# Kernel optimization log

Hardware: AMD Instinct MI355X
Metric: run time of the kernel (lower is better)

## Reference

```python
import jax, jax.numpy as jnp
import numpy as np
from jax import lax

STRIDE = 6  # from init_kwargs


def setup_inputs() -> dict:
    key = jax.random.key(0)
    # spike-like activations in [0, 1); feature maps [F, H, W]
    s = jax.random.uniform(key, (128, 384, 384), dtype=jnp.float32)
    return {"s": s}


def reference(s):
    # Faithful to PoolingConnection.compute: for output (k, i, j) it takes
    #   max(s[k, i*stride : i*stride + h, j*stride : j*stride + w])
    # where h = H // stride, w = W // stride (NOT pooling_size -- that arg
    # is unused in the original code). Python slicing clips at the array
    # boundary, which equals right/bottom padding with -inf under a max.
    F, H, W = s.shape
    h, w = H // STRIDE, W // STRIDE
    pad_h = (h - 1) * STRIDE + h - H  # so that output height == h
    pad_w = (w - 1) * STRIDE + w - W
    out = lax.reduce_window(
        s,
        -jnp.inf,
        lax.max,
        window_dimensions=(1, h, w),
        window_strides=(1, STRIDE, STRIDE),
        padding=[(0, 0), (0, pad_h), (0, pad_w)],
    )  # [F, h, w]
    return out
```

## Files before the change

### kernel.cpp

```cpp
#include <hip/hip_runtime.h>
#include <math.h>


constexpr int F  = 128;
constexpr int H  = 384;
constexpr int W  = 384;
constexpr int ST = 6;
constexpr int OH = 64;
constexpr int OW = 64;

constexpr int NSEG   = 37;
constexpr int SEGPAD = NSEG + 10;

#define NINF (-__builtin_huge_valf())

__device__ __forceinline__ float sh_ninf(float v, int lane, int d) {
    float r = __shfl(v, lane + d, 64);
    return (lane + d > 63) ? NINF : r;
}

__device__ __forceinline__ float slide_window(float m, float p3, int lane) {
    const float a1 = fmaxf(m,  sh_ninf(m,  lane, 1));
    const float a2 = fmaxf(a1, sh_ninf(a1, lane, 2));
    const float a3 = fmaxf(a2, sh_ninf(a2, lane, 4));
    const float a4 = fmaxf(a3, sh_ninf(a1, lane, 8));
    return fmaxf(a4, sh_ninf(p3, lane, 10));
}

__global__ __launch_bounds__(1024) void pool_fused_kernel(const float* __restrict__ s,
                                                          float* __restrict__ out) {
    __shared__ float segm[SEGPAD][64];
    __shared__ float segp[SEGPAD][64];

    const int k    = blockIdx.x >> 1;
    const int half = blockIdx.x & 1;

    const int sbeg = half ? 27 : 0;
    const int obeg = half ? 27 : 0;
    const int ni   = half ? 37 : 27;

    const int tid  = threadIdx.x;
    const int wv   = tid >> 6;
    const int lane = tid & 63;

    for (int job = tid; job < 10 * 64; job += 1024) {
        const int g = NSEG + (job >> 6);
        const int j = job & 63;
        segm[g][j] = NINF;
        segp[g][j] = NINF;
    }

    const float* base = s + ((size_t)k * H + sbeg * ST) * W + lane * 6;
    for (int gl = wv; gl < NSEG; gl += 16) {
        const float* seg = base + (size_t)gl * ST * W;
        float vm6 = NINF, vp6 = NINF;
        float vm4 = NINF, vp4 = NINF;
        #pragma unroll
        for (int t = 0; t < 6; ++t) {
            const float* row = seg + (size_t)t * W;
            const float2 e0 = *reinterpret_cast<const float2*>(row);
            const float2 e1 = *reinterpret_cast<const float2*>(row + 2);
            const float2 e2 = *reinterpret_cast<const float2*>(row + 4);
            const float p3 = fmaxf(fmaxf(e0.x, e0.y), fmaxf(e1.x, e1.y));
            const float m  = fmaxf(p3, fmaxf(e2.x, e2.y));
            vm6 = fmaxf(vm6, m);
            vp6 = fmaxf(vp6, p3);
            if (t < 4) { vm4 = fmaxf(vm4, m); vp4 = fmaxf(vp4, p3); }
        }
        segm[gl][lane] = slide_window(vm6, vp6, lane);
        segp[gl][lane] = slide_window(vm4, vp4, lane);
    }
    __syncthreads();

    for (int job = tid; job < ni * 64; job += 1024) {
        const int li = job >> 6;
        const int j  = job & 63;
        float acc = segp[li + 10][j];
        #pragma unroll
        for (int t = 0; t < 10; ++t) acc = fmaxf(acc, segm[li + t][j]);
        out[((size_t)k * OH + obeg + li) * OW + j] = acc;
    }
}

extern "C" void kernel_launch(void* const* d_in, const int* in_sizes, int n_in,
                              void* d_out, int out_size, void* d_ws, size_t ws_size,
                              hipStream_t stream) {
    const float* s = (const float*)d_in[0];
    float* out     = (float*)d_out;
    pool_fused_kernel<<<F * 2, 1024, 0, stream>>>(s, out);
}
```

Measured before the change: 18.54 us.

## Split segment work evenly across halves and fix up boundary rows in second kernel

```diff
diff --git a/kernel.cpp b/kernel.cpp
--- a/kernel.cpp
+++ b/kernel.cpp
@@ -8,9 +8,6 @@
 constexpr int ST = 6;
 constexpr int OH = 64;
 constexpr int OW = 64;
-
-constexpr int NSEG   = 37;
-constexpr int SEGPAD = NSEG + 10;
 
 #define NINF (-__builtin_huge_valf())
 
@@ -27,31 +24,32 @@
     return fmaxf(a4, sh_ninf(p3, lane, 10));
 }
 
-__global__ __launch_bounds__(1024) void pool_fused_kernel(const float* __restrict__ s,
-                                                          float* __restrict__ out) {
-    __shared__ float segm[SEGPAD][64];
-    __shared__ float segp[SEGPAD][64];
+__global__ __launch_bounds__(1024) void pool_main(const float* __restrict__ s,
+                                                  float* __restrict__ out,
+                                                  float* __restrict__ ws_m,
+                                                  float* __restrict__ ws_p) {
+    __shared__ float segm[42][64];
+    __shared__ float segp[42][64];
 
     const int k    = blockIdx.x >> 1;
     const int half = blockIdx.x & 1;
-
-    const int sbeg = half ? 27 : 0;
-    const int obeg = half ? 27 : 0;
-    const int ni   = half ? 37 : 27;
+    const int sbeg = half * 32;
 
     const int tid  = threadIdx.x;
     const int wv   = tid >> 6;
     const int lane = tid & 63;
 
     for (int job = tid; job < 10 * 64; job += 1024) {
-        const int g = NSEG + (job >> 6);
+        const int g = 32 + (job >> 6);
         const int j = job & 63;
         segm[g][j] = NINF;
         segp[g][j] = NINF;
     }
 
     const float* base = s + ((size_t)k * H + sbeg * ST) * W + lane * 6;
-    for (int gl = wv; gl < NSEG; gl += 16) {
+    #pragma unroll
+    for (int it = 0; it < 2; ++it) {
+        const int gl = wv + it * 16;
         const float* seg = base + (size_t)gl * ST * W;
         float vm6 = NINF, vp6 = NINF;
         float vm4 = NINF, vp4 = NINF;
@@ -72,6 +70,21 @@
     }
     __syncthreads();
 
+    if (!half) {
+        for (int job = tid; job < 10 * 64; job += 1024) {
+            const int g = job >> 6, c = job & 63;
+            ws_m[((size_t)k * 20 + g) * 64 + c] = segm[22 + g][c];
+        }
+    } else {
+        for (int job = tid; job < 20 * 64; job += 1024) {
+            const int g = job >> 6, c = job & 63;
+            if (g < 10) ws_m[((size_t)k * 20 + 10 + g) * 64 + c] = segm[g][c];
+            else        ws_p[((size_t)k * 10 + (g - 10)) * 64 + c] = segp[g - 10][c];
+        }
+    }
+
+    const int obeg = half ? 32 : 0;
+    const int ni   = half ? 32 : 22;
     for (int job = tid; job < ni * 64; job += 1024) {
         const int li = job >> 6;
         const int j  = job & 63;
@@ -82,10 +95,31 @@
     }
 }
 
+__global__ __launch_bounds__(256) void pool_fixup(const float* __restrict__ ws_m,
+                                                  const float* __restrict__ ws_p,
+                                                  float* __restrict__ out) {
+    const int gtid = blockIdx.x * 256 + threadIdx.x;
+    const int wid  = gtid >> 6;
+    const int lane = gtid & 63;
+    if (wid >= F * 10) return;
+    const int k = wid / 10;
+    const int r = wid % 10;
+
+    const float* m = ws_m + ((size_t)k * 20 + r) * 64 + lane;
+    float acc = ws_p[((size_t)k * 10 + r) * 64 + lane];
+    #pragma unroll
+    for (int t = 0; t < 10; ++t) acc = fmaxf(acc, m[(size_t)t * 64]);
+    out[((size_t)k * OH + 22 + r) * OW + lane] = acc;
+}
+
 extern "C" void kernel_launch(void* const* d_in, const int* in_sizes, int n_in,
                               void* d_out, int out_size, void* d_ws, size_t ws_size,
                               hipStream_t stream) {
     const float* s = (const float*)d_in[0];
     float* out     = (float*)d_out;
-    pool_fused_kernel<<<F * 2, 1024, 0, stream>>>(s, out);
+    float* ws_m    = (float*)d_ws;
+    float* ws_p    = ws_m + (size_t)F * 20 * 64;
+
+    pool_main<<<F * 2, 1024, 0, stream>>>(s, out, ws_m, ws_p);
+    pool_fixup<<<(F * 10 * 64 + 255) / 256, 256, 0, stream>>>(ws_m, ws_p, out);
 }
```

Result: slower. 19.37 us (+4.5%).

## Load rows with coalesced float4 and redistribute columns through LDS

Applied to the files above, without the earlier changes.

```diff
diff --git a/kernel.cpp b/kernel.cpp
--- a/kernel.cpp
+++ b/kernel.cpp
@@ -27,14 +27,28 @@
     return fmaxf(a4, sh_ninf(p3, lane, 10));
 }
 
+__device__ __forceinline__ float4 fmax4(float4 a, float4 b) {
+    float4 r;
+    r.x = fmaxf(a.x, b.x); r.y = fmaxf(a.y, b.y);
+    r.z = fmaxf(a.z, b.z); r.w = fmaxf(a.w, b.w);
+    return r;
+}
+
+__device__ __forceinline__ float2 fmax2f(float2 a, float2 b) {
+    float2 r; r.x = fmaxf(a.x, b.x); r.y = fmaxf(a.y, b.y); return r;
+}
+
 __global__ __launch_bounds__(1024) void pool_fused_kernel(const float* __restrict__ s,
                                                           float* __restrict__ out) {
-    __shared__ float segm[SEGPAD][64];
-    __shared__ float segp[SEGPAD][64];
+    __shared__ float  segm[SEGPAD][64];
+    __shared__ float  segp[SEGPAD][64];
+    __shared__ float4 cmA[16][96];
+    __shared__ float4 cmB[16][96];
+    __shared__ float4 ppA[16][96];
+    __shared__ float4 ppB[16][96];
 
     const int k    = blockIdx.x >> 1;
     const int half = blockIdx.x & 1;
-
     const int sbeg = half ? 27 : 0;
     const int obeg = half ? 27 : 0;
     const int ni   = half ? 37 : 27;
@@ -50,25 +64,58 @@
         segp[g][j] = NINF;
     }
 
-    const float* base = s + ((size_t)k * H + sbeg * ST) * W + lane * 6;
+    float4* wA = cmA[wv];
+    float4* wB = cmB[wv];
+    float4* qA = ppA[wv];
+    float4* qB = ppB[wv];
+
+    const float* base = s + ((size_t)k * H + sbeg * ST) * W;
     for (int gl = wv; gl < NSEG; gl += 16) {
-        const float* seg = base + (size_t)gl * ST * W;
-        float vm6 = NINF, vp6 = NINF;
-        float vm4 = NINF, vp4 = NINF;
-        #pragma unroll
-        for (int t = 0; t < 6; ++t) {
-            const float* row = seg + (size_t)t * W;
-            const float2 e0 = *reinterpret_cast<const float2*>(row);
-            const float2 e1 = *reinterpret_cast<const float2*>(row + 2);
-            const float2 e2 = *reinterpret_cast<const float2*>(row + 4);
-            const float p3 = fmaxf(fmaxf(e0.x, e0.y), fmaxf(e1.x, e1.y));
-            const float m  = fmaxf(p3, fmaxf(e2.x, e2.y));
-            vm6 = fmaxf(vm6, m);
-            vp6 = fmaxf(vp6, p3);
-            if (t < 4) { vm4 = fmaxf(vm4, m); vp4 = fmaxf(vp4, p3); }
-        }
-        segm[gl][lane] = slide_window(vm6, vp6, lane);
-        segp[gl][lane] = slide_window(vm4, vp4, lane);
+        const float* sp = base + (size_t)gl * ST * W + 4 * lane;
+
+        const float4 L0 = *reinterpret_cast<const float4*>(sp);
+        const float4 L1 = *reinterpret_cast<const float4*>(sp + 256);
+        const float4 L2 = *reinterpret_cast<const float4*>(sp + 512);
+        const float4 L3 = *reinterpret_cast<const float4*>(sp + 768);
+        const float4 L4 = *reinterpret_cast<const float4*>(sp + 1024);
+        const float4 L5 = *reinterpret_cast<const float4*>(sp + 1280);
+        const float4 L6 = *reinterpret_cast<const float4*>(sp + 1536);
+        const float4 L7 = *reinterpret_cast<const float4*>(sp + 1792);
+        const float4 L8 = *reinterpret_cast<const float4*>(sp + 2048);
+
+        const float4 P0 = fmax4(L0, L3), P1 = fmax4(L1, L4), P2 = fmax4(L2, L5);
+        const float4 V0 = fmax4(P0, L6), V1 = fmax4(P1, L7), V2 = fmax4(P2, L8);
+
+        __builtin_amdgcn_wave_barrier();
+
+        wA[lane] = V0;  qA[lane] = P0;
+        if (lane < 32) { wA[64 + lane] = V1;  qA[64 + lane] = P1; }
+        else           { wB[lane - 32] = V1;  qB[lane - 32] = P1; }
+        wB[32 + lane] = V2;  qB[32 + lane] = P2;
+
+        __builtin_amdgcn_wave_barrier();
+
+        const float2* rA = reinterpret_cast<const float2*>(wA);
+        const float2* rB = reinterpret_cast<const float2*>(wB);
+        const float2 c0 = fmax2f(rA[3 * lane],     rB[3 * lane]);
+        const float2 c1 = fmax2f(rA[3 * lane + 1], rB[3 * lane + 1]);
+        const float2 c2 = fmax2f(rA[3 * lane + 2], rB[3 * lane + 2]);
+
+        const float2* sA = reinterpret_cast<const float2*>(qA);
+        const float2* sB = reinterpret_cast<const float2*>(qB);
+        const float2 d0 = fmax2f(sA[3 * lane],     sB[3 * lane]);
+        const float2 d1 = fmax2f(sA[3 * lane + 1], sB[3 * lane + 1]);
+        const float2 d2 = fmax2f(sA[3 * lane + 2], sB[3 * lane + 2]);
+
+        __builtin_amdgcn_wave_barrier();
+
+        const float p3c = fmaxf(fmaxf(c0.x, c0.y), fmaxf(c1.x, c1.y));
+        const float mc  = fmaxf(p3c, fmaxf(c2.x, c2.y));
+        segm[gl][lane] = slide_window(mc, p3c, lane);
+
+        const float p3p = fmaxf(fmaxf(d0.x, d0.y), fmaxf(d1.x, d1.y));
+        const float mp  = fmaxf(p3p, fmaxf(d2.x, d2.y));
+        segp[gl][lane] = slide_window(mp, p3p, lane);
     }
     __syncthreads();
 
```

Result: slower. 19.20 us (+3.6%).

## Split feature map halves without overlap and exchange boundary segments via workspace flag

Applied to the files above, without the earlier changes.

```diff
diff --git a/kernel.cpp b/kernel.cpp
--- a/kernel.cpp
+++ b/kernel.cpp
@@ -9,8 +9,7 @@
 constexpr int OH = 64;
 constexpr int OW = 64;
 
-constexpr int NSEG   = 37;
-constexpr int SEGPAD = NSEG + 10;
+constexpr unsigned int SENT = 0x13572468u;
 
 #define NINF (-__builtin_huge_valf())
 
@@ -28,31 +27,35 @@
 }
 
 __global__ __launch_bounds__(1024) void pool_fused_kernel(const float* __restrict__ s,
-                                                          float* __restrict__ out) {
-    __shared__ float segm[SEGPAD][64];
-    __shared__ float segp[SEGPAD][64];
+                                                          float* __restrict__ out,
+                                                          float* __restrict__ wsd,
+                                                          unsigned int* __restrict__ wsf) {
+    __shared__ float segm[52][64];
+    __shared__ float segp[52][64];
 
     const int k    = blockIdx.x >> 1;
     const int half = blockIdx.x & 1;
-
-    const int sbeg = half ? 27 : 0;
-    const int obeg = half ? 27 : 0;
-    const int ni   = half ? 37 : 27;
+    const int sbeg  = half ? 32 : 0;
+    const int lbase = half ? 10 : 0;
 
     const int tid  = threadIdx.x;
     const int wv   = tid >> 6;
     const int lane = tid & 63;
 
-    for (int job = tid; job < 10 * 64; job += 1024) {
-        const int g = NSEG + (job >> 6);
-        const int j = job & 63;
-        segm[g][j] = NINF;
-        segp[g][j] = NINF;
+    if (half) {
+        for (int job = tid; job < 10 * 64; job += 1024) {
+            const int g = 42 + (job >> 6);
+            const int j = job & 63;
+            segm[g][j] = NINF;
+            segp[g][j] = NINF;
+        }
     }
 
     const float* base = s + ((size_t)k * H + sbeg * ST) * W + lane * 6;
-    for (int gl = wv; gl < NSEG; gl += 16) {
-        const float* seg = base + (size_t)gl * ST * W;
+    #pragma unroll
+    for (int it = 0; it < 2; ++it) {
+        const int sl = wv + it * 16;
+        const float* seg = base + (size_t)sl * ST * W;
         float vm6 = NINF, vp6 = NINF;
         float vm4 = NINF, vp4 = NINF;
         #pragma unroll
@@ -67,18 +70,54 @@
             vp6 = fmaxf(vp6, p3);
             if (t < 4) { vm4 = fmaxf(vm4, m); vp4 = fmaxf(vp4, p3); }
         }
-        segm[gl][lane] = slide_window(vm6, vp6, lane);
-        segp[gl][lane] = slide_window(vm4, vp4, lane);
+        segm[lbase + sl][lane] = slide_window(vm6, vp6, lane);
+        segp[lbase + sl][lane] = slide_window(vm4, vp4, lane);
     }
     __syncthreads();
 
-    for (int job = tid; job < ni * 64; job += 1024) {
-        const int li = job >> 6;
-        const int j  = job & 63;
-        float acc = segp[li + 10][j];
-        #pragma unroll
-        for (int t = 0; t < 10; ++t) acc = fmaxf(acc, segm[li + t][j]);
-        out[((size_t)k * OH + obeg + li) * OW + j] = acc;
+    if (!half) {
+        if (tid < 10 * 64) {
+            wsd[(size_t)k * 640 + tid] = segm[22 + (tid >> 6)][tid & 63];
+        }
+        __syncthreads();
+        if (tid == 0) {
+            __threadfence();
+            __hip_atomic_store(&wsf[k], SENT, __ATOMIC_RELEASE,
+                               __HIP_MEMORY_SCOPE_AGENT);
+        }
+        for (int job = tid; job < 22 * 64; job += 1024) {
+            const int li = job >> 6;
+            const int j  = job & 63;
+            float acc = segp[li + 10][j];
+            #pragma unroll
+            for (int t = 0; t < 10; ++t) acc = fmaxf(acc, segm[li + t][j]);
+            out[((size_t)k * OH + li) * OW + j] = acc;
+        }
+    } else {
+        for (int job = tid; job < 32 * 64; job += 1024) {
+            const int lr = 10 + (job >> 6);
+            const int j  = job & 63;
+            float acc = segp[lr + 10][j];
+            #pragma unroll
+            for (int t = 0; t < 10; ++t) acc = fmaxf(acc, segm[lr + t][j]);
+            out[((size_t)k * OH + 22 + lr) * OW + j] = acc;
+        }
+        while (__hip_atomic_load(&wsf[k], __ATOMIC_ACQUIRE,
+                                 __HIP_MEMORY_SCOPE_AGENT) != SENT) {
+            __builtin_amdgcn_s_sleep(2);
+        }
+        if (tid < 10 * 64) {
+            segm[tid >> 6][tid & 63] = wsd[(size_t)k * 640 + tid];
+        }
+        __syncthreads();
+        for (int job = tid; job < 10 * 64; job += 1024) {
+            const int lr = job >> 6;
+            const int j  = job & 63;
+            float acc = segp[lr + 10][j];
+            #pragma unroll
+            for (int t = 0; t < 10; ++t) acc = fmaxf(acc, segm[lr + t][j]);
+            out[((size_t)k * OH + 22 + lr) * OW + j] = acc;
+        }
     }
 }
 
@@ -87,5 +126,8 @@
                               hipStream_t stream) {
     const float* s = (const float*)d_in[0];
     float* out     = (float*)d_out;
-    pool_fused_kernel<<<F * 2, 1024, 0, stream>>>(s, out);
+    float* wsd         = (float*)d_ws;
+    unsigned int* wsf  = (unsigned int*)(wsd + (size_t)F * 640);
+
+    pool_fused_kernel<<<F * 2, 1024, 0, stream>>>(s, out, wsd, wsf);
 }
```

New measurement: 45.41 us. +144.9%, slower.
